# Optimization experiments

Measured on AMD Instinct MI355X. Metric: run time of the kernel, lower is better.

The kernel has to match this reference:

```python
import jax, jax.numpy as jnp
import numpy as np

B, T, D, H = 2, 2048, 1024, 16
DH = D // H
THETA = 10000.0
MAX_SEQ_LEN = 2048


def setup_inputs() -> dict:
    key = jax.random.key(0)
    kx, kqkv, ko = jax.random.split(key, 3)
    # trunc_normal init matching the torch Linear (std=sqrt(2/(fan_in+fan_out)), clipped at 3 sigma)
    sigma_qkv = (2.0 / (D + 3 * D)) ** 0.5
    sigma_o = (2.0 / (D + D)) ** 0.5
    W_qkv = jax.random.truncated_normal(kqkv, -3.0, 3.0, (3 * D, D), jnp.float32) * sigma_qkv
    W_o = jax.random.truncated_normal(ko, -3.0, 3.0, (D, D), jnp.float32) * sigma_o
    # RoPE caches: angles[t, i] = t / theta^(2i/d_k)
    dims = jnp.arange(0, DH, 2, dtype=jnp.float32)
    inv_freq = 1.0 / (THETA ** (dims / DH))  # [DH/2]
    angles = jnp.arange(MAX_SEQ_LEN, dtype=jnp.float32)[:, None] * inv_freq[None, :]  # [T, DH/2]
    return {
        "x": jax.random.normal(kx, (B, T, D), jnp.float32),
        "token_positions": jnp.arange(T, dtype=jnp.int64 if jax.config.jax_enable_x64 else jnp.int32),
        "W_qkv": W_qkv,
        "W_o": W_o,
        "cos_cached": jnp.cos(angles),
        "sin_cached": jnp.sin(angles),
    }


def _apply_rope(x, cos, sin):
    # x: [b, h, t, dh]; cos/sin: [t, dh/2] broadcast over (b, h)
    x1 = x[..., 0::2]
    x2 = x[..., 1::2]
    r1 = x1 * cos - x2 * sin
    r2 = x1 * sin + x2 * cos
    # interleave back: (.., dh/2, 2) -> (.., dh)
    return jnp.stack([r1, r2], axis=-1).reshape(x.shape)


def reference(x, token_positions, W_qkv, W_o, cos_cached, sin_cached):
    b, t, d = x.shape
    qkv = jnp.einsum("btd,ed->bte", x, W_qkv)  # [b, t, 3d]
    q, k, v = jnp.split(qkv, 3, axis=-1)

    def to_heads(z):
        return z.reshape(b, t, H, DH).transpose(0, 2, 1, 3)  # [b, h, t, dh]

    q, k, v = to_heads(q), to_heads(k), to_heads(v)

    cos = cos_cached[token_positions]  # [t, dh/2]
    sin = sin_cached[token_positions]
    q = _apply_rope(q, cos, sin)
    k = _apply_rope(k, cos, sin)

    scale = 1.0 / jnp.sqrt(jnp.asarray(DH, x.dtype))
    scores = jnp.einsum("bhqd,bhkd->bhqk", q, k) * scale  # full TxT (naive, matches source)
    causal = jnp.tril(jnp.ones((t, t), dtype=bool))  # [t, t]
    scores = jnp.where(causal[None, None, :, :], scores, -jnp.inf)
    attn = jax.nn.softmax(scores, axis=-1)
    out = jnp.einsum("bhqk,bhkd->bhqd", attn, v)  # [b, h, t, dh]
    out = out.transpose(0, 2, 1, 3).reshape(b, t, d)
    return jnp.einsum("btd,ed->bte", out, W_o)
```

## Files before the change

kernel.cpp:

```cpp
#include <hip/hip_runtime.h>
#include <hip/hip_bf16.h>
#include <stdint.h>

#define Bn  2
#define Tn  2048
#define Dn  1024
#define Hn  16
#define DHn 64
#define QSCALE 0.1803368801111204f

typedef unsigned short u16;
typedef __attribute__((ext_vector_type(8))) short s16x8;
typedef __attribute__((ext_vector_type(8))) unsigned short u16x8;
typedef __attribute__((ext_vector_type(4))) unsigned short u16x4;
typedef __attribute__((ext_vector_type(4))) float f32x4;

#define MFMA(a, b, c) __builtin_amdgcn_mfma_f32_16x16x32_bf16((a), (b), (c), 0, 0, 0)

__device__ __forceinline__ u16 f2bf(float f) {
  union { __hip_bfloat16 b; u16 u; } c;
  c.b = __float2bfloat16(f);
  return c.u;
}
__device__ __forceinline__ float bf2f(u16 u) {
  union { u16 u; __hip_bfloat16 b; } c;
  c.u = u;
  return __bfloat162float(c.b);
}

__device__ __forceinline__ void lds16(void* lds, const void* g) {
  __builtin_amdgcn_global_load_lds((__attribute__((address_space(1))) void*)(g),
                                   (__attribute__((address_space(3))) void*)(lds), 16, 0, 0);
}

__global__ __launch_bounds__(256) void k_cvt2(const float* __restrict__ s0, int n0,
                                              const float* __restrict__ s1, int n1,
                                              u16* __restrict__ dst) {
  int i = blockIdx.x * blockDim.x + threadIdx.x;
  const int stride = gridDim.x * blockDim.x;
  const int nt = n0 + n1;
  for (; i < nt; i += stride) {
    float4 v = (i < n0) ? ((const float4*)s0)[i] : ((const float4*)s1)[i - n0];
    u16x4 o;
    o[0] = f2bf(v.x); o[1] = f2bf(v.y); o[2] = f2bf(v.z); o[3] = f2bf(v.w);
    ((u16x4*)dst)[i] = o;
  }
}

__global__ __launch_bounds__(256) void k_cvt(const float* __restrict__ src,
                                             u16* __restrict__ dst, int n4) {
  int i = blockIdx.x * blockDim.x + threadIdx.x;
  const int stride = gridDim.x * blockDim.x;
  for (; i < n4; i += stride) {
    float4 v = ((const float4*)src)[i];
    u16x4 o;
    o[0] = f2bf(v.x); o[1] = f2bf(v.y); o[2] = f2bf(v.z); o[3] = f2bf(v.w);
    ((u16x4*)dst)[i] = o;
  }
}

__global__ __launch_bounds__(256) void k_qkv(
    const u16* __restrict__ xb, const u16* __restrict__ wb,
    const int* __restrict__ tokpos,
    const float* __restrict__ cosc, const float* __restrict__ sinc,
    u16* __restrict__ qb, u16* __restrict__ kb, u16* __restrict__ vtb)
{
  __shared__ u16 smem[17408];
  const int tid  = threadIdx.x;
  const int bcol = blockIdx.x;
  const int brow = blockIdx.y;
  const int lane = tid & 63, w = tid >> 6;
  const int wr = w >> 1, wc = w & 1;
  const int l15 = lane & 15, l4 = lane >> 4;
  const int lrow = lane >> 2;
  const int gsw  = (((lane & 3) ^ ((lrow >> 1) & 3)) * 8);
  const int rsw  = (l15 >> 1) & 3;

  const u16* xrow = xb + (size_t)(brow * 128) * 1024;
  const u16* wrow = wb + (size_t)(bcol * 128) * 1024;

  f32x4 acc[4][4] = {};

  {
    const int r0 = w * 32;
    lds16(&smem[r0 * 32],              xrow + (size_t)(r0 + lrow) * 1024 + gsw);
    lds16(&smem[(r0 + 16) * 32],       xrow + (size_t)(r0 + 16 + lrow) * 1024 + gsw);
    lds16(&smem[8192 + r0 * 32],       wrow + (size_t)(r0 + lrow) * 1024 + gsw);
    lds16(&smem[8192 + (r0 + 16) * 32],wrow + (size_t)(r0 + 16 + lrow) * 1024 + gsw);
  }

  for (int kt = 0; kt < 32; ++kt) {
    const int cur = kt & 1;
    const u16* Asb = smem + cur * 4096;
    const u16* Bsb = smem + 8192 + cur * 4096;
    if (kt < 31) {
      u16* Asn = smem + (cur ^ 1) * 4096;
      u16* Bsn = smem + 8192 + (cur ^ 1) * 4096;
      const int k1 = (kt + 1) * 32;
      const int r0 = w * 32;
      lds16(&Asn[r0 * 32],        xrow + (size_t)(r0 + lrow) * 1024 + k1 + gsw);
      lds16(&Asn[(r0 + 16) * 32], xrow + (size_t)(r0 + 16 + lrow) * 1024 + k1 + gsw);
      lds16(&Bsn[r0 * 32],        wrow + (size_t)(r0 + lrow) * 1024 + k1 + gsw);
      lds16(&Bsn[(r0 + 16) * 32], wrow + (size_t)(r0 + 16 + lrow) * 1024 + k1 + gsw);
      asm volatile("s_waitcnt vmcnt(4)" ::: "memory");
    } else {
      asm volatile("s_waitcnt vmcnt(0)" ::: "memory");
    }
    __builtin_amdgcn_s_barrier();
    __builtin_amdgcn_sched_barrier(0);
    __builtin_amdgcn_s_setprio(1);
    {
      const int gr = (l4 ^ rsw) * 8;
      s16x8 af[4], bf[4];
#pragma unroll
      for (int m = 0; m < 4; ++m)
        af[m] = *(const s16x8*)&Asb[(wr * 64 + m * 16 + l15) * 32 + gr];
#pragma unroll
      for (int n = 0; n < 4; ++n)
        bf[n] = *(const s16x8*)&Bsb[(wc * 64 + n * 16 + l15) * 32 + gr];
#pragma unroll
      for (int m = 0; m < 4; ++m)
#pragma unroll
        for (int n = 0; n < 4; ++n)
          acc[m][n] = MFMA(af[m], bf[n], acc[m][n]);
    }
    __builtin_amdgcn_s_setprio(0);
    __builtin_amdgcn_sched_barrier(0);
    __builtin_amdgcn_s_barrier();
  }

#pragma unroll
  for (int m = 0; m < 4; ++m)
#pragma unroll
    for (int n = 0; n < 4; ++n)
#pragma unroll
      for (int r = 0; r < 4; ++r)
        smem[(wr * 64 + m * 16 + l4 * 4 + r) * 136 + wc * 64 + n * 16 + l15] =
            f2bf(acc[m][n][r]);
  __syncthreads();

  if (bcol < 16) {
    u16* dst; float sc;
    if (bcol < 8) { dst = qb; sc = QSCALE; } else { dst = kb; sc = 1.0f; }
#pragma unroll
    for (int ph = 0; ph < 8; ++ph) {
      const int task = ph * 256 + tid;
      const int lr   = task >> 4;
      const int cg   = task & 15;
      const int rowg = brow * 128 + lr;
      const int b = rowg >> 11, t = rowg & 2047;
      const int rem = (bcol * 128 + cg * 8) & 1023;
      const int h = rem >> 6, dh0 = rem & 63;
      u16x8 v = *(const u16x8*)&smem[lr * 136 + cg * 8];
      const int pos = tokpos[t];
      const float4 cv = *(const float4*)&cosc[pos * 32 + (dh0 >> 1)];
      const float4 sv = *(const float4*)&sinc[pos * 32 + (dh0 >> 1)];
      const float cc[4] = {cv.x, cv.y, cv.z, cv.w};
      const float ss[4] = {sv.x, sv.y, sv.z, sv.w};
      u16x8 o;
#pragma unroll
      for (int p = 0; p < 4; ++p) {
        const float x1 = bf2f(v[2 * p]), x2 = bf2f(v[2 * p + 1]);
        o[2 * p]     = f2bf((x1 * cc[p] - x2 * ss[p]) * sc);
        o[2 * p + 1] = f2bf((x1 * ss[p] + x2 * cc[p]) * sc);
      }
      *(u16x8*)(dst + ((size_t)(b * Hn + h) * Tn + t) * DHn + dh0) = o;
    }
  } else {
    const int b  = (brow * 128) >> 11;
    const int t0 = (brow * 128) & 2047;
#pragma unroll
    for (int ph = 0; ph < 8; ++ph) {
      const int task = ph * 256 + tid;
      const int col = task & 127;
      const int tg  = task >> 7;
      const int h  = 2 * (bcol - 16) + (col >> 6);
      const int dh = col & 63;
      u16x8 v;
#pragma unroll
      for (int j = 0; j < 8; ++j) v[j] = smem[(tg * 8 + j) * 136 + col];
      *(u16x8*)(vtb + ((size_t)(b * Hn + h) * DHn + dh) * Tn + t0 + tg * 8) = v;
    }
  }
}

__global__ __launch_bounds__(512) void k_attn(
    const u16* __restrict__ qbuf, const u16* __restrict__ kbuf,
    const u16* __restrict__ vtb, u16* __restrict__ ob)
{
  __shared__ u16 Ks[2][64][64];
  __shared__ u16 Vs[2][64][64];
  __shared__ u16 Ps[8][16][64];

  const int tid  = threadIdx.x;
  const int lane = tid & 63, w = tid >> 6;
  const int l15 = lane & 15, l4 = lane >> 4;
  const int lrow = lane >> 3;
  const int gsw  = ((lane & 7) ^ (lane >> 3)) * 8;
  const int rsw  = l15 & 7;

  const int lin = blockIdx.x;
  const int bh  = lin & 31;
  const int a   = (lin >> 5) & 7, rb = lin >> 8;
  const int qblk = rb ? (15 - a) : a;
  const int b = bh >> 4, h = bh & 15;

  const u16* Qh = qbuf + (size_t)bh * Tn * DHn;
  const u16* Kh = kbuf + (size_t)bh * Tn * DHn;
  const u16* Vh = vtb  + (size_t)bh * DHn * Tn;

  const int q0 = qblk * 128 + w * 16;
  const int ntiles = 2 * qblk + 2;

  const s16x8 qf0 = *(const s16x8*)(Qh + (size_t)(q0 + l15) * 64 + l4 * 8);
  const s16x8 qf1 = *(const s16x8*)(Qh + (size_t)(q0 + l15) * 64 + 32 + l4 * 8);

  const s16x8 onesv = {(short)0x3F80, (short)0x3F80, (short)0x3F80, (short)0x3F80,
                       (short)0x3F80, (short)0x3F80, (short)0x3F80, (short)0x3F80};

  f32x4 o[4] = {};
  f32x4 o5 = {};
  float m = -3.0e38f;

  {
    const int r0 = w * 8;
    lds16(&Ks[0][r0][0], Kh + (size_t)(r0 + lrow) * 64 + gsw);
    lds16(&Vs[0][r0][0], Vh + (size_t)(r0 + lrow) * Tn + gsw);
  }

  for (int it = 0; it < ntiles; ++it) {
    const int buf = it & 1;
    if (it + 1 < ntiles) {
      const int nb = buf ^ 1;
      const int kv1 = (it + 1) * 64;
      const int r0 = w * 8;
      lds16(&Ks[nb][r0][0], Kh + (size_t)(kv1 + r0 + lrow) * 64 + gsw);
      lds16(&Vs[nb][r0][0], Vh + (size_t)(r0 + lrow) * Tn + kv1 + gsw);
      asm volatile("s_waitcnt vmcnt(2)" ::: "memory");
    } else {
      asm volatile("s_waitcnt vmcnt(0)" ::: "memory");
    }
    __builtin_amdgcn_s_barrier();
    __builtin_amdgcn_sched_barrier(0);

    const int kv0 = it * 64;
    const bool active = (kv0 <= q0 + 15);
    if (active) {
      f32x4 s[4] = {};
      __builtin_amdgcn_s_setprio(1);
#pragma unroll
      for (int ks = 0; ks < 2; ++ks) {
        const s16x8 qf = ks ? qf1 : qf0;
        const int gr = ((ks * 4 + l4) ^ rsw) * 8;
#pragma unroll
        for (int hh = 0; hh < 4; ++hh) {
          const s16x8 kf = *(const s16x8*)&Ks[buf][hh * 16 + l15][gr];
          s[hh] = MFMA(kf, qf, s[hh]);
        }
      }
      __builtin_amdgcn_s_setprio(0);

      if (kv0 + 63 > q0) {
        const int kvb = kv0 + l4 * 4;
        const int qg  = q0 + l15;
#pragma unroll
        for (int hh = 0; hh < 4; ++hh)
#pragma unroll
          for (int rr = 0; rr < 4; ++rr)
            if (kvb + hh * 16 + rr > qg) s[hh][rr] = -3.0e38f;
      }

      const float a0 = fmaxf(fmaxf(s[0][0], s[0][1]), s[0][2]);
      const float a1 = fmaxf(fmaxf(s[0][3], s[1][0]), s[1][1]);
      const float a2 = fmaxf(fmaxf(s[1][2], s[1][3]), s[2][0]);
      const float a3 = fmaxf(fmaxf(s[2][1], s[2][2]), s[2][3]);
      const float a4 = fmaxf(fmaxf(s[3][0], s[3][1]), s[3][2]);
      float tmax = fmaxf(fmaxf(fmaxf(a0, a1), fmaxf(a2, a3)), fmaxf(a4, s[3][3]));
      tmax = fmaxf(tmax, __shfl_xor(tmax, 16));
      tmax = fmaxf(tmax, __shfl_xor(tmax, 32));

      if (__any(tmax > m + 8.0f)) {
        const float mn    = fmaxf(m, tmax);
        const float alpha = __builtin_amdgcn_exp2f(m - mn);
        m = mn;
#pragma unroll
        for (int n = 0; n < 4; ++n)
#pragma unroll
          for (int rr = 0; rr < 4; ++rr) o[n][rr] *= alpha;
#pragma unroll
        for (int rr = 0; rr < 4; ++rr) o5[rr] *= alpha;
      }

#pragma unroll
      for (int hh = 0; hh < 4; ++hh) {
        u16x4 pk;
#pragma unroll
        for (int rr = 0; rr < 4; ++rr)
          pk[rr] = f2bf(__builtin_amdgcn_exp2f(s[hh][rr] - m));
        const int pg = ((hh << 1) + (l4 >> 1)) ^ rsw;
        *(u16x4*)&Ps[w][l15][pg * 8 + (l4 & 1) * 4] = pk;
      }

      const s16x8 pf0 = *(const s16x8*)&Ps[w][l15][(l4 ^ rsw) * 8];
      const s16x8 pf1 = *(const s16x8*)&Ps[w][l15][((4 + l4) ^ rsw) * 8];

      __builtin_amdgcn_s_setprio(1);
#pragma unroll
      for (int n = 0; n < 4; ++n) {
        const int g0 = (l4 ^ rsw) * 8, g1 = ((4 + l4) ^ rsw) * 8;
        const s16x8 vf0 = *(const s16x8*)&Vs[buf][n * 16 + l15][g0];
        const s16x8 vf1 = *(const s16x8*)&Vs[buf][n * 16 + l15][g1];
        o[n] = MFMA(vf0, pf0, o[n]);
        o[n] = MFMA(vf1, pf1, o[n]);
      }
      o5 = MFMA(onesv, pf0, o5);
      o5 = MFMA(onesv, pf1, o5);
      __builtin_amdgcn_s_setprio(0);
    }
    __builtin_amdgcn_sched_barrier(0);
    __builtin_amdgcn_s_barrier();
  }

  const float inv = 1.0f / o5[0];
  const int t = q0 + l15;
#pragma unroll
  for (int n = 0; n < 4; ++n) {
    u16x4 ov;
#pragma unroll
    for (int rr = 0; rr < 4; ++rr) ov[rr] = f2bf(o[n][rr] * inv);
    *(u16x4*)(ob + (size_t)(b * Tn + t) * Dn + h * 64 + n * 16 + l4 * 4) = ov;
  }
}

__global__ __launch_bounds__(256) void k_out(
    const u16* __restrict__ ob, const u16* __restrict__ wob,
    float* __restrict__ out)
{
  __shared__ u16 smem[24576];
  const int tid  = threadIdx.x;
  const int bcol = blockIdx.x;
  const int brow = blockIdx.y;
  const int lane = tid & 63, w = tid >> 6;
  const int wr = w >> 1, wc = w & 1;
  const int l15 = lane & 15, l4 = lane >> 4;
  const int lrow = lane >> 3;
  const int gsw  = ((lane & 7) ^ (lane >> 3)) * 8;
  const int rsw  = l15 & 7;

  f32x4 acc[4][2] = {};

#pragma unroll
  for (int c = 0; c < 4; ++c) {
    const int r0 = w * 32 + c * 8;
    lds16(&smem[r0 * 64], ob + (size_t)(brow * 128 + r0 + lrow) * 1024 + gsw);
  }
#pragma unroll
  for (int c = 0; c < 2; ++c) {
    const int r0 = w * 16 + c * 8;
    lds16(&smem[16384 + r0 * 64], wob + (size_t)(bcol * 64 + r0 + lrow) * 1024 + gsw);
  }

  for (int kt = 0; kt < 16; ++kt) {
    const int cur = kt & 1;
    const u16* Asb = smem + cur * 8192;
    const u16* Bsb = smem + 16384 + cur * 4096;
    if (kt < 15) {
      u16* Asn = smem + (cur ^ 1) * 8192;
      u16* Bsn = smem + 16384 + (cur ^ 1) * 4096;
      const int k1 = (kt + 1) * 64;
#pragma unroll
      for (int c = 0; c < 4; ++c) {
        const int r0 = w * 32 + c * 8;
        lds16(&Asn[r0 * 64], ob + (size_t)(brow * 128 + r0 + lrow) * 1024 + k1 + gsw);
      }
#pragma unroll
      for (int c = 0; c < 2; ++c) {
        const int r0 = w * 16 + c * 8;
        lds16(&Bsn[r0 * 64], wob + (size_t)(bcol * 64 + r0 + lrow) * 1024 + k1 + gsw);
      }
      asm volatile("s_waitcnt vmcnt(6)" ::: "memory");
    } else {
      asm volatile("s_waitcnt vmcnt(0)" ::: "memory");
    }
    __builtin_amdgcn_s_barrier();
    __builtin_amdgcn_sched_barrier(0);
    __builtin_amdgcn_s_setprio(1);
#pragma unroll
    for (int kk = 0; kk < 64; kk += 32) {
      const int gc = (kk >> 3) + l4;
      s16x8 af[4], bf[2];
#pragma unroll
      for (int m = 0; m < 4; ++m)
        af[m] = *(const s16x8*)&Asb[(wr * 64 + m * 16 + l15) * 64 + ((gc ^ rsw) * 8)];
#pragma unroll
      for (int n = 0; n < 2; ++n)
        bf[n] = *(const s16x8*)&Bsb[(wc * 32 + n * 16 + l15) * 64 + ((gc ^ rsw) * 8)];
#pragma unroll
      for (int m = 0; m < 4; ++m)
#pragma unroll
        for (int n = 0; n < 2; ++n)
          acc[m][n] = MFMA(af[m], bf[n], acc[m][n]);
    }
    __builtin_amdgcn_s_setprio(0);
    __builtin_amdgcn_sched_barrier(0);
    __builtin_amdgcn_s_barrier();
  }

#pragma unroll
  for (int m = 0; m < 4; ++m) {
    const int rowb = brow * 128 + wr * 64 + m * 16 + l4 * 4;
#pragma unroll
    for (int n = 0; n < 2; ++n) {
      const int colg = bcol * 64 + wc * 32 + n * 16 + l15;
#pragma unroll
      for (int r = 0; r < 4; ++r)
        out[(size_t)(rowb + r) * 1024 + colg] = acc[m][n][r];
    }
  }
}

extern "C" void kernel_launch(void* const* d_in, const int* in_sizes, int n_in,
                              void* d_out, int out_size, void* d_ws, size_t ws_size,
                              hipStream_t stream) {
  const float* x      = (const float*)d_in[0];
  const int*   tokpos = (const int*)d_in[1];
  const float* wqkv   = (const float*)d_in[2];
  const float* wo     = (const float*)d_in[3];
  const float* cosc   = (const float*)d_in[4];
  const float* sinc   = (const float*)d_in[5];
  float* out = (float*)d_out;

  u16* xb    = (u16*)d_ws;
  u16* wqkvb = xb + (size_t)Bn * Tn * Dn;
  u16* qb    = wqkvb + (size_t)3 * Dn * Dn;
  u16* kb    = qb + (size_t)Bn * Tn * Dn;
  u16* vtb   = kb + (size_t)Bn * Tn * Dn;
  u16* ob    = xb;
  u16* wob   = wqkvb;

  dim3 blk(256);
  k_cvt2<<<dim3(2048), blk, 0, stream>>>(x, (Bn * Tn * Dn) / 4,
                                         wqkv, (3 * Dn * Dn) / 4, xb);

  k_qkv<<<dim3(24, 32), blk, 0, stream>>>(xb, wqkvb, tokpos, cosc, sinc, qb, kb, vtb);

  k_cvt<<<dim3(1024), blk, 0, stream>>>(wo, wob, (Dn * Dn) / 4);

  k_attn<<<dim3(512), dim3(512), 0, stream>>>(qb, kb, vtb, ob);

  k_out<<<dim3(16, 32), blk, 0, stream>>>(ob, wob, out);
}
```

Before: 105.4 us.

## Widen attention KV tiles to 128 keys and drop per-wave active check

Doubles the KV tile processed per loop iteration from 64 to 128 keys, halving the number of barrier-synchronized iterations and making the QK^T phase issue eight MFMAs per k-step. The V tile layout becomes 64x128 with a 16-way XOR swizzle. The softmax/PV stage is split into two 64-key phases that reuse the per-wave P buffer. The per-wave skip of fully masked tiles is removed, so waves on the diagonal now compute and mask some extra work. LDS use doubles and register pressure rises.

```diff
diff --git a/kernel.cpp b/kernel.cpp
--- a/kernel.cpp
+++ b/kernel.cpp
@@ -188,16 +188,15 @@
     const u16* __restrict__ qbuf, const u16* __restrict__ kbuf,
     const u16* __restrict__ vtb, u16* __restrict__ ob)
 {
-  __shared__ u16 Ks[2][64][64];
-  __shared__ u16 Vs[2][64][64];
+  __shared__ u16 Ks[2][128][64];
+  __shared__ u16 Vs[2][64][128];
   __shared__ u16 Ps[8][16][64];
 
   const int tid  = threadIdx.x;
   const int lane = tid & 63, w = tid >> 6;
   const int l15 = lane & 15, l4 = lane >> 4;
-  const int lrow = lane >> 3;
-  const int gsw  = ((lane & 7) ^ (lane >> 3)) * 8;
   const int rsw  = l15 & 7;
+  const int kgsw = ((lane & 7) ^ (lane >> 3)) * 8;
 
   const int lin = blockIdx.x;
   const int bh  = lin & 31;
@@ -210,7 +209,7 @@
   const u16* Vh = vtb  + (size_t)bh * DHn * Tn;
 
   const int q0 = qblk * 128 + w * 16;
-  const int ntiles = 2 * qblk + 2;
+  const int ntiles = qblk + 1;
 
   const s16x8 qf0 = *(const s16x8*)(Qh + (size_t)(q0 + l15) * 64 + l4 * 8);
   const s16x8 qf1 = *(const s16x8*)(Qh + (size_t)(q0 + l15) * 64 + 32 + l4 * 8);
@@ -222,94 +221,107 @@
   f32x4 o5 = {};
   float m = -3.0e38f;
 
-  {
-    const int r0 = w * 8;
-    lds16(&Ks[0][r0][0], Kh + (size_t)(r0 + lrow) * 64 + gsw);
-    lds16(&Vs[0][r0][0], Vh + (size_t)(r0 + lrow) * Tn + gsw);
+  const int vl4 = lane >> 4;
+
+#pragma unroll
+  for (int i = 0; i < 2; ++i) {
+    const int kr = w * 16 + i * 8;
+    lds16(&Ks[0][kr][0], Kh + (size_t)(kr + (lane >> 3)) * 64 + kgsw);
+    const int vr = w * 8 + i * 4;
+    const int vrow = vr + vl4;
+    lds16(&Vs[0][vr][0], Vh + (size_t)vrow * Tn + ((lane & 15) ^ (vrow & 15)) * 8);
   }
 
   for (int it = 0; it < ntiles; ++it) {
     const int buf = it & 1;
     if (it + 1 < ntiles) {
       const int nb = buf ^ 1;
-      const int kv1 = (it + 1) * 64;
-      const int r0 = w * 8;
-      lds16(&Ks[nb][r0][0], Kh + (size_t)(kv1 + r0 + lrow) * 64 + gsw);
-      lds16(&Vs[nb][r0][0], Vh + (size_t)(r0 + lrow) * Tn + kv1 + gsw);
-      asm volatile("s_waitcnt vmcnt(2)" ::: "memory");
+      const int kv1 = (it + 1) * 128;
+#pragma unroll
+      for (int i = 0; i < 2; ++i) {
+        const int kr = w * 16 + i * 8;
+        lds16(&Ks[nb][kr][0], Kh + (size_t)(kv1 + kr + (lane >> 3)) * 64 + kgsw);
+        const int vr = w * 8 + i * 4;
+        const int vrow = vr + vl4;
+        lds16(&Vs[nb][vr][0],
+              Vh + (size_t)vrow * Tn + kv1 + ((lane & 15) ^ (vrow & 15)) * 8);
+      }
+      asm volatile("s_waitcnt vmcnt(4)" ::: "memory");
     } else {
       asm volatile("s_waitcnt vmcnt(0)" ::: "memory");
     }
     __builtin_amdgcn_s_barrier();
     __builtin_amdgcn_sched_barrier(0);
 
-    const int kv0 = it * 64;
-    const bool active = (kv0 <= q0 + 15);
-    if (active) {
-      f32x4 s[4] = {};
-      __builtin_amdgcn_s_setprio(1);
-#pragma unroll
-      for (int ks = 0; ks < 2; ++ks) {
-        const s16x8 qf = ks ? qf1 : qf0;
-        const int gr = ((ks * 4 + l4) ^ rsw) * 8;
-#pragma unroll
-        for (int hh = 0; hh < 4; ++hh) {
-          const s16x8 kf = *(const s16x8*)&Ks[buf][hh * 16 + l15][gr];
-          s[hh] = MFMA(kf, qf, s[hh]);
-        }
-      }
-      __builtin_amdgcn_s_setprio(0);
-
-      if (kv0 + 63 > q0) {
-        const int kvb = kv0 + l4 * 4;
-        const int qg  = q0 + l15;
-#pragma unroll
-        for (int hh = 0; hh < 4; ++hh)
-#pragma unroll
-          for (int rr = 0; rr < 4; ++rr)
-            if (kvb + hh * 16 + rr > qg) s[hh][rr] = -3.0e38f;
-      }
-
-      const float a0 = fmaxf(fmaxf(s[0][0], s[0][1]), s[0][2]);
-      const float a1 = fmaxf(fmaxf(s[0][3], s[1][0]), s[1][1]);
-      const float a2 = fmaxf(fmaxf(s[1][2], s[1][3]), s[2][0]);
-      const float a3 = fmaxf(fmaxf(s[2][1], s[2][2]), s[2][3]);
-      const float a4 = fmaxf(fmaxf(s[3][0], s[3][1]), s[3][2]);
-      float tmax = fmaxf(fmaxf(fmaxf(a0, a1), fmaxf(a2, a3)), fmaxf(a4, s[3][3]));
-      tmax = fmaxf(tmax, __shfl_xor(tmax, 16));
-      tmax = fmaxf(tmax, __shfl_xor(tmax, 32));
-
-      if (__any(tmax > m + 8.0f)) {
-        const float mn    = fmaxf(m, tmax);
-        const float alpha = __builtin_amdgcn_exp2f(m - mn);
-        m = mn;
-#pragma unroll
-        for (int n = 0; n < 4; ++n)
-#pragma unroll
-          for (int rr = 0; rr < 4; ++rr) o[n][rr] *= alpha;
-#pragma unroll
-        for (int rr = 0; rr < 4; ++rr) o5[rr] *= alpha;
-      }
-
-#pragma unroll
-      for (int hh = 0; hh < 4; ++hh) {
+    const int kv0 = it * 128;
+
+    f32x4 s[8] = {};
+    __builtin_amdgcn_s_setprio(1);
+#pragma unroll
+    for (int ks = 0; ks < 2; ++ks) {
+      const s16x8 qf = ks ? qf1 : qf0;
+      const int gr = ((ks * 4 + l4) ^ rsw) * 8;
+#pragma unroll
+      for (int qd = 0; qd < 8; ++qd) {
+        const s16x8 kf = *(const s16x8*)&Ks[buf][qd * 16 + l15][gr];
+        s[qd] = MFMA(kf, qf, s[qd]);
+      }
+    }
+    __builtin_amdgcn_s_setprio(0);
+
+    if (it == ntiles - 1) {
+      const int kvb = kv0 + l4 * 4;
+      const int qg  = q0 + l15;
+#pragma unroll
+      for (int qd = 0; qd < 8; ++qd)
+#pragma unroll
+        for (int rr = 0; rr < 4; ++rr)
+          if (kvb + qd * 16 + rr > qg) s[qd][rr] = -3.0e38f;
+    }
+
+    float qm[8];
+#pragma unroll
+    for (int qd = 0; qd < 8; ++qd)
+      qm[qd] = fmaxf(fmaxf(s[qd][0], s[qd][1]), fmaxf(s[qd][2], s[qd][3]));
+    float tmax = fmaxf(fmaxf(fmaxf(qm[0], qm[1]), fmaxf(qm[2], qm[3])),
+                       fmaxf(fmaxf(qm[4], qm[5]), fmaxf(qm[6], qm[7])));
+    tmax = fmaxf(tmax, __shfl_xor(tmax, 16));
+    tmax = fmaxf(tmax, __shfl_xor(tmax, 32));
+
+    if (__any(tmax > m + 8.0f)) {
+      const float mn    = fmaxf(m, tmax);
+      const float alpha = __builtin_amdgcn_exp2f(m - mn);
+      m = mn;
+#pragma unroll
+      for (int n = 0; n < 4; ++n)
+#pragma unroll
+        for (int rr = 0; rr < 4; ++rr) o[n][rr] *= alpha;
+#pragma unroll
+      for (int rr = 0; rr < 4; ++rr) o5[rr] *= alpha;
+    }
+
+#pragma unroll
+    for (int ph = 0; ph < 2; ++ph) {
+#pragma unroll
+      for (int hl = 0; hl < 4; ++hl) {
+        const int qd = ph * 4 + hl;
         u16x4 pk;
 #pragma unroll
         for (int rr = 0; rr < 4; ++rr)
-          pk[rr] = f2bf(__builtin_amdgcn_exp2f(s[hh][rr] - m));
-        const int pg = ((hh << 1) + (l4 >> 1)) ^ rsw;
+          pk[rr] = f2bf(__builtin_amdgcn_exp2f(s[qd][rr] - m));
+        const int pg = ((hl << 1) + (l4 >> 1)) ^ rsw;
         *(u16x4*)&Ps[w][l15][pg * 8 + (l4 & 1) * 4] = pk;
       }
-
       const s16x8 pf0 = *(const s16x8*)&Ps[w][l15][(l4 ^ rsw) * 8];
       const s16x8 pf1 = *(const s16x8*)&Ps[w][l15][((4 + l4) ^ rsw) * 8];
 
       __builtin_amdgcn_s_setprio(1);
 #pragma unroll
       for (int n = 0; n < 4; ++n) {
-        const int g0 = (l4 ^ rsw) * 8, g1 = ((4 + l4) ^ rsw) * 8;
-        const s16x8 vf0 = *(const s16x8*)&Vs[buf][n * 16 + l15][g0];
-        const s16x8 vf1 = *(const s16x8*)&Vs[buf][n * 16 + l15][g1];
+        const s16x8 vf0 =
+            *(const s16x8*)&Vs[buf][n * 16 + l15][((ph * 8 + l4) ^ l15) * 8];
+        const s16x8 vf1 =
+            *(const s16x8*)&Vs[buf][n * 16 + l15][((ph * 8 + 4 + l4) ^ l15) * 8];
         o[n] = MFMA(vf0, pf0, o[n]);
         o[n] = MFMA(vf1, pf1, o[n]);
       }
```

Result: faster. 99.50 us (-5.6%).
